# Kernel optimization log

Measured on AMD Instinct MI355X. Metric: run time of the kernel, lower is better.

The kernel has to match this reference:

```python
import jax, jax.numpy as jnp
from jax import lax
import numpy as np

B, T, H, A, C = 32, 4096, 512, 512, 32  # batch, enc frames, hidden, attn_size, conv_size


def setup_inputs() -> dict:
    key = jax.random.key(0)
    ks = jax.random.split(key, 10)
    return {
        "decoder_output": jax.random.normal(ks[0], (B, 1, H), jnp.float32),
        "encoder_outputs": jax.random.normal(ks[1], (B, T, H), jnp.float32),
        "last_alignment": jax.random.uniform(ks[2], (B, T), jnp.float32),
        "conv_w": jax.random.normal(ks[3], (C, 1, 3), jnp.float32) * 0.1,   # Conv1d(1->C, k=3)
        "conv_b": jax.random.normal(ks[4], (C,), jnp.float32) * 0.1,
        "W": jax.random.normal(ks[5], (A, H), jnp.float32) * (1.0 / np.sqrt(H)),
        "V": jax.random.normal(ks[6], (A, H), jnp.float32) * (1.0 / np.sqrt(H)),
        "U": jax.random.normal(ks[7], (A, C), jnp.float32) * (1.0 / np.sqrt(C)),
        "b": jax.random.uniform(ks[8], (A,), jnp.float32, -0.1, 0.1),
        "w": jax.random.normal(ks[9], (A,), jnp.float32) * (1.0 / np.sqrt(A)),
    }


def reference(decoder_output, encoder_outputs, last_alignment, conv_w, conv_b, W, V, U, b, w):
    # location conv: [B,1,T] -> [B,C,T], kernel 3, padding 1
    conv = lax.conv_general_dilated(
        last_alignment[:, None, :], conv_w,
        window_strides=(1,), padding=[(1, 1)],
        dimension_numbers=("NCH", "OIH", "NCH"))
    conv_feat = (conv + conv_b[None, :, None]).transpose(0, 2, 1)  # [B,T,C]

    dec_proj = jnp.einsum("blh,ah->bla", decoder_output, W)        # [B,1,A]
    enc_proj = jnp.einsum("bth,ah->bta", encoder_outputs, V)       # [B,T,A]
    loc_proj = jnp.einsum("btc,ac->bta", conv_feat, U)             # [B,T,A]

    scores = jnp.einsum("bta,a->bt", jnp.tanh(dec_proj + enc_proj + loc_proj + b), w)  # [B,T]
    alignment = jax.nn.softmax(scores, axis=-1)                    # [B,T]
    output = jnp.einsum("bt,bth->bh", alignment, encoder_outputs)  # [B,H]
    return output, alignment
```

## Files before the change

kernel.cpp:

```cpp
#include <hip/hip_runtime.h>
#include <hip/hip_bf16.h>

#define B_ 32
#define T_ 4096
#define H_ 512
#define A_ 512
#define C_ 32
#define KTOT 544
#define NKS  (KTOT / 32)
#define TT   64
#define NCH  (T_ / TT)

typedef float f32x4 __attribute__((ext_vector_type(4)));
typedef __bf16 bf16x8 __attribute__((ext_vector_type(8)));

__device__ inline float fast_tanh(float x) {
    float t = __expf(2.0f * x);
    return 1.0f - 2.0f / (t + 1.0f);
}

__device__ __forceinline__ void async16(const void* g, void* l) {
    __builtin_amdgcn_global_load_lds(
        (const __attribute__((address_space(1))) unsigned int*)g,
        (__attribute__((address_space(3))) unsigned int*)l, 16, 0, 0);
}

__global__ __launch_bounds__(256) void prep_kernel(
    const float* __restrict__ dec, const float* __restrict__ W,
    const float* __restrict__ bvec, const float* __restrict__ V,
    const float* __restrict__ U,
    float* __restrict__ dpb, __bf16* __restrict__ Vsall) {
    int id = blockIdx.x * 256 + threadIdx.x;
    const int N1 = B_ * A_;
    const int N2 = A_ * H_;
    if (id < N1) {
        int b = id / A_, a = id % A_;
        const float* dr = dec + b * H_;
        const float* wr = W + (size_t)a * H_;
        float s = 0.f;
        #pragma unroll 8
        for (int h = 0; h < H_; ++h) s += dr[h] * wr[h];
        dpb[id] = s + bvec[a];
    } else if (id < N1 + N2) {
        int e = id - N1;
        int a = e >> 9, k = e & 511;
        Vsall[((k >> 3) * A_ + a) * 8 + (k & 7)] = (__bf16)V[(size_t)a * H_ + k];
    } else {
        int e = id - N1 - N2;
        int a = e >> 5, c = e & 31;
        int k = H_ + c;
        Vsall[((k >> 3) * A_ + a) * 8 + (k & 7)] = (__bf16)U[a * C_ + c];
    }
}

__global__ __launch_bounds__(512) void scores_mfma(
    const float* __restrict__ enc, const float* __restrict__ align,
    const float* __restrict__ conv_w, const float* __restrict__ conv_b,
    const __bf16* __restrict__ Vsall, const float* __restrict__ dpb,
    const float* __restrict__ wvec, float* __restrict__ scores,
    float* __restrict__ ml_buf, float* __restrict__ u_buf) {
    const int bx = blockIdx.x;
    const int t0 = bx * TT;
    const int b  = blockIdx.y;
    const int tid = threadIdx.x;
    const int lane = tid & 63, wid = tid >> 6;
    const int row0 = lane & 15;
    const int kg   = lane >> 4;
    const int wq   = wid & 3;
    const int wr   = wid >> 2;
    const int wcol = wq * 128;

    __shared__ char smem[73728];
    float* spart = (float*)smem;
    float* eL    = (float*)(smem + 2048);
    float* mbox  = (float*)(smem + 2560);

    const float* encb = enc + ((size_t)b * T_ + t0) * H_;
    const int arow = tid >> 2, akgl = tid & 3;

    {
        __bf16* bdst = (__bf16*)(smem + 8192);
        #pragma unroll
        for (int i = 0; i < 4; ++i) {
            int u = i * 512 + tid;
            async16(Vsall + u * 8, bdst + u * 8);
        }
    }
    if (tid < 256) {
        const float* p = encb + arow * H_ + akgl * 8;
        f32x4 lo = *reinterpret_cast<const f32x4*>(p);
        f32x4 hi = *reinterpret_cast<const f32x4*>(p + 4);
        bf16x8 v;
        v[0] = (__bf16)lo.x; v[1] = (__bf16)lo.y; v[2] = (__bf16)lo.z; v[3] = (__bf16)lo.w;
        v[4] = (__bf16)hi.x; v[5] = (__bf16)hi.y; v[6] = (__bf16)hi.z; v[7] = (__bf16)hi.w;
        int g = tid ^ ((tid >> 4) & 7);
        *reinterpret_cast<bf16x8*>((__bf16*)smem + g * 8) = v;
    }
    __syncthreads();

    f32x4 acc[2][8];
    #pragma unroll
    for (int m = 0; m < 2; ++m)
        #pragma unroll
        for (int n = 0; n < 8; ++n) acc[m][n] = (f32x4){0.f, 0.f, 0.f, 0.f};

    int cur = 0;
    for (int ks = 0; ks < NKS; ++ks) {
        __bf16* Acur = (__bf16*)(smem + (cur ? 4096 : 0));
        __bf16* Anxt = (__bf16*)(smem + (cur ? 0 : 4096));
        __bf16* Bcur = (__bf16*)(smem + 8192 + (cur ? 32768 : 0));
        __bf16* Bnxt = (__bf16*)(smem + 8192 + (cur ? 0 : 32768));

        f32x4 alo, ahi;
        bool stage = (ks + 1 < NKS);
        bool conv_step = (ks + 1 == NKS - 1);
        if (stage) {
            const __bf16* vchunk = Vsall + (size_t)(ks + 1) * (4 * A_ * 8);
            #pragma unroll
            for (int i = 0; i < 4; ++i) {
                int u = i * 512 + tid;
                async16(vchunk + u * 8, Bnxt + u * 8);
            }
            if (tid < 256 && !conv_step) {
                const float* p = encb + arow * H_ + (ks + 1) * 32 + akgl * 8;
                alo = *reinterpret_cast<const f32x4*>(p);
                ahi = *reinterpret_cast<const f32x4*>(p + 4);
            }
        }

        bf16x8 afrag[2];
        #pragma unroll
        for (int m = 0; m < 2; ++m) {
            int row = wr * 32 + m * 16 + row0;
            int u = row * 4 + kg;
            int g = u ^ ((u >> 4) & 7);
            afrag[m] = *reinterpret_cast<const bf16x8*>(Acur + g * 8);
        }
        const __bf16* bp = Bcur + kg * (A_ * 8);
        #pragma unroll
        for (int n = 0; n < 8; ++n) {
            bf16x8 bfrag = *reinterpret_cast<const bf16x8*>(bp + (wcol + n * 16 + row0) * 8);
            acc[0][n] = __builtin_amdgcn_mfma_f32_16x16x32_bf16(afrag[0], bfrag, acc[0][n], 0, 0, 0);
            acc[1][n] = __builtin_amdgcn_mfma_f32_16x16x32_bf16(afrag[1], bfrag, acc[1][n], 0, 0, 0);
        }

        if (stage && tid < 256) {
            bf16x8 v;
            if (!conv_step) {
                v[0] = (__bf16)alo.x; v[1] = (__bf16)alo.y; v[2] = (__bf16)alo.z; v[3] = (__bf16)alo.w;
                v[4] = (__bf16)ahi.x; v[5] = (__bf16)ahi.y; v[6] = (__bf16)ahi.z; v[7] = (__bf16)ahi.w;
            } else {
                int t = t0 + arow;
                float x0 = (t > 0) ? align[b * T_ + t - 1] : 0.f;
                float x1 = align[b * T_ + t];
                float x2 = (t + 1 < T_) ? align[b * T_ + t + 1] : 0.f;
                #pragma unroll
                for (int e = 0; e < 8; ++e) {
                    int c = akgl * 8 + e;
                    v[e] = (__bf16)(conv_b[c] + conv_w[c * 3 + 0] * x0
                                  + conv_w[c * 3 + 1] * x1 + conv_w[c * 3 + 2] * x2);
                }
            }
            int g = tid ^ ((tid >> 4) & 7);
            *reinterpret_cast<bf16x8*>(Anxt + g * 8) = v;
        }
        __syncthreads();
        cur ^= 1;
    }

    float dval[8], wv[8];
    #pragma unroll
    for (int n = 0; n < 8; ++n) {
        int a = wcol + n * 16 + row0;
        dval[n] = dpb[b * A_ + a];
        wv[n]   = wvec[a];
    }
    #pragma unroll
    for (int m = 0; m < 2; ++m) {
        float rs[4] = {0.f, 0.f, 0.f, 0.f};
        #pragma unroll
        for (int n = 0; n < 8; ++n) {
            #pragma unroll
            for (int j = 0; j < 4; ++j) {
                float x = acc[m][n][j] + dval[n];
                rs[j] += fast_tanh(x) * wv[n];
            }
        }
        #pragma unroll
        for (int j = 0; j < 4; ++j) {
            float v = rs[j];
            v += __shfl_xor(v, 1);
            v += __shfl_xor(v, 2);
            v += __shfl_xor(v, 4);
            v += __shfl_xor(v, 8);
            if (row0 == 0) spart[wq * TT + wr * 32 + m * 16 + kg * 4 + j] = v;
        }
    }
    __syncthreads();

    if (tid < TT) {
        float s = spart[0 * TT + tid] + spart[1 * TT + tid]
                + spart[2 * TT + tid] + spart[3 * TT + tid];
        scores[b * T_ + t0 + tid] = s;
        float mx = s;
        #pragma unroll
        for (int off = 32; off >= 1; off >>= 1) mx = fmaxf(mx, __shfl_xor(mx, off));
        float e = __expf(s - mx);
        eL[tid] = e;
        float l = e;
        #pragma unroll
        for (int off = 32; off >= 1; off >>= 1) l += __shfl_xor(l, off);
        if (tid == 0) {
            mbox[0] = mx;
            ml_buf[((size_t)b * NCH + bx) * 2 + 0] = mx;
            ml_buf[((size_t)b * NCH + bx) * 2 + 1] = l;
        }
    }
    __syncthreads();
    {
        float u0 = 0.f, u1 = 0.f, u2 = 0.f, u3 = 0.f;
        const float* ep = encb + tid;
        #pragma unroll 4
        for (int t = 0; t < TT; t += 4) {
            u0 += eL[t]     * ep[(size_t)t * H_];
            u1 += eL[t + 1] * ep[(size_t)(t + 1) * H_];
            u2 += eL[t + 2] * ep[(size_t)(t + 2) * H_];
            u3 += eL[t + 3] * ep[(size_t)(t + 3) * H_];
        }
        u_buf[((size_t)b * NCH + bx) * H_ + tid] = (u0 + u1) + (u2 + u3);
    }
}

__global__ __launch_bounds__(256) void softmax_k(
    const float* __restrict__ scores, float* __restrict__ out_align) {
    int b = blockIdx.x;
    int tid = threadIdx.x;
    __shared__ float redm[4];
    __shared__ float reds[4];
    float local[16];
    float mx = -1e30f;
    #pragma unroll
    for (int i = 0; i < 16; ++i) {
        float s = scores[b * T_ + tid + i * 256];
        local[i] = s;
        mx = fmaxf(mx, s);
    }
    for (int off = 32; off >= 1; off >>= 1) mx = fmaxf(mx, __shfl_xor(mx, off));
    if ((tid & 63) == 0) redm[tid >> 6] = mx;
    __syncthreads();
    mx = fmaxf(fmaxf(redm[0], redm[1]), fmaxf(redm[2], redm[3]));
    float sum = 0.f;
    #pragma unroll
    for (int i = 0; i < 16; ++i) { local[i] = __expf(local[i] - mx); sum += local[i]; }
    for (int off = 32; off >= 1; off >>= 1) sum += __shfl_xor(sum, off);
    if ((tid & 63) == 0) reds[tid >> 6] = sum;
    __syncthreads();
    sum = reds[0] + reds[1] + reds[2] + reds[3];
    float inv = 1.0f / sum;
    #pragma unroll
    for (int i = 0; i < 16; ++i)
        out_align[b * T_ + tid + i * 256] = local[i] * inv;
}

__global__ __launch_bounds__(512) void combine2_k(
    const float* __restrict__ ml_buf, const float* __restrict__ u_buf,
    float* __restrict__ out) {
    int b = blockIdx.x;
    int h = threadIdx.x;
    __shared__ float wsh[NCH];
    __shared__ float dsh[1];
    if (h < NCH) {
        float m = ml_buf[((size_t)b * NCH + h) * 2];
        float mb = m;
        #pragma unroll
        for (int off = 32; off >= 1; off >>= 1) mb = fmaxf(mb, __shfl_xor(mb, off));
        float w = __expf(m - mb);
        wsh[h] = w;
        float d = w * ml_buf[((size_t)b * NCH + h) * 2 + 1];
        #pragma unroll
        for (int off = 32; off >= 1; off >>= 1) d += __shfl_xor(d, off);
        if (h == 0) dsh[0] = d;
    }
    __syncthreads();
    float acc = 0.f;
    #pragma unroll 4
    for (int c = 0; c < NCH; ++c)
        acc += wsh[c] * u_buf[((size_t)b * NCH + c) * H_ + h];
    out[b * H_ + h] = acc / dsh[0];
}

extern "C" void kernel_launch(void* const* d_in, const int* in_sizes, int n_in,
                              void* d_out, int out_size, void* d_ws, size_t ws_size,
                              hipStream_t stream) {
    const float* dec    = (const float*)d_in[0];
    const float* enc    = (const float*)d_in[1];
    const float* align  = (const float*)d_in[2];
    const float* conv_w = (const float*)d_in[3];
    const float* conv_b = (const float*)d_in[4];
    const float* W      = (const float*)d_in[5];
    const float* V      = (const float*)d_in[6];
    const float* U      = (const float*)d_in[7];
    const float* bvec   = (const float*)d_in[8];
    const float* wvec   = (const float*)d_in[9];
    float* out       = (float*)d_out;
    float* out_align = out + B_ * H_;

    char* ws = (char*)d_ws;
    float*  dpb    = (float*)(ws);
    float*  scores = (float*)(ws + (64 << 10));
    float*  ml_buf = (float*)(ws + (576 << 10));
    float*  u_buf  = (float*)(ws + (592 << 10));
    __bf16* Vsall  = (__bf16*)(ws + (592 << 10) + (4 << 20));

    prep_kernel<<<(B_ * A_ + A_ * H_ + A_ * C_) / 256, 256, 0, stream>>>(
        dec, W, bvec, V, U, dpb, Vsall);
    scores_mfma<<<dim3(T_ / TT, B_), 512, 0, stream>>>(enc, align, conv_w, conv_b,
                                                       Vsall, dpb, wvec, scores,
                                                       ml_buf, u_buf);
    softmax_k<<<B_, 256, 0, stream>>>(scores, out_align);
    combine2_k<<<B_, 512, 0, stream>>>(ml_buf, u_buf, out);
}
```

Before: 166.9 us.

## Keep all bf16 encoder tiles in LDS and reuse them for weighted sum

The A-tile staging buffers are no longer double-buffered. Each k-step's bf16 encoder slice now gets its own LDS region, so the whole 64x512 tile stays resident. The closing context accumulation reads encoder values from LDS instead of re-reading fp32 encoder rows from global memory. This removes a second global pass over the encoder block, but LDS per block grows to about 136KB, which cuts occupancy to one block per CU, and the context sum now uses bf16-rounded encoder values.

```diff
diff --git a/kernel.cpp b/kernel.cpp
--- a/kernel.cpp
+++ b/kernel.cpp
@@ -10,6 +10,11 @@
 #define NKS  (KTOT / 32)
 #define TT   64
 #define NCH  (T_ / TT)
+
+#define LDS_B0   69632
+#define LDS_SP   135168
+#define LDS_EL   136192
+#define LDS_SZ   136448
 
 typedef float f32x4 __attribute__((ext_vector_type(4)));
 typedef __bf16 bf16x8 __attribute__((ext_vector_type(8)));
@@ -70,16 +75,16 @@
     const int wr   = wid >> 2;
     const int wcol = wq * 128;
 
-    __shared__ char smem[73728];
-    float* spart = (float*)smem;
-    float* eL    = (float*)(smem + 2048);
-    float* mbox  = (float*)(smem + 2560);
+    __shared__ char smem[LDS_SZ];
+    float* spart = (float*)(smem + LDS_SP);
+    float* eL    = (float*)(smem + LDS_EL);
 
     const float* encb = enc + ((size_t)b * T_ + t0) * H_;
     const int arow = tid >> 2, akgl = tid & 3;
+    const int ag = tid ^ ((tid >> 4) & 7);
 
     {
-        __bf16* bdst = (__bf16*)(smem + 8192);
+        __bf16* bdst = (__bf16*)(smem + LDS_B0);
         #pragma unroll
         for (int i = 0; i < 4; ++i) {
             int u = i * 512 + tid;
@@ -93,8 +98,7 @@
         bf16x8 v;
         v[0] = (__bf16)lo.x; v[1] = (__bf16)lo.y; v[2] = (__bf16)lo.z; v[3] = (__bf16)lo.w;
         v[4] = (__bf16)hi.x; v[5] = (__bf16)hi.y; v[6] = (__bf16)hi.z; v[7] = (__bf16)hi.w;
-        int g = tid ^ ((tid >> 4) & 7);
-        *reinterpret_cast<bf16x8*>((__bf16*)smem + g * 8) = v;
+        *reinterpret_cast<bf16x8*>(smem + ag * 16) = v;
     }
     __syncthreads();
 
@@ -104,12 +108,11 @@
         #pragma unroll
         for (int n = 0; n < 8; ++n) acc[m][n] = (f32x4){0.f, 0.f, 0.f, 0.f};
 
-    int cur = 0;
     for (int ks = 0; ks < NKS; ++ks) {
-        __bf16* Acur = (__bf16*)(smem + (cur ? 4096 : 0));
-        __bf16* Anxt = (__bf16*)(smem + (cur ? 0 : 4096));
-        __bf16* Bcur = (__bf16*)(smem + 8192 + (cur ? 32768 : 0));
-        __bf16* Bnxt = (__bf16*)(smem + 8192 + (cur ? 0 : 32768));
+        char* Acur = smem + ks * 4096;
+        char* Anxt = smem + (ks + 1) * 4096;
+        char* Bcur = smem + LDS_B0 + (ks & 1) * 32768;
+        char* Bnxt = smem + LDS_B0 + ((ks + 1) & 1) * 32768;
 
         f32x4 alo, ahi;
         bool stage = (ks + 1 < NKS);
@@ -119,7 +122,7 @@
             #pragma unroll
             for (int i = 0; i < 4; ++i) {
                 int u = i * 512 + tid;
-                async16(vchunk + u * 8, Bnxt + u * 8);
+                async16(vchunk + u * 8, (__bf16*)Bnxt + u * 8);
             }
             if (tid < 256 && !conv_step) {
                 const float* p = encb + arow * H_ + (ks + 1) * 32 + akgl * 8;
@@ -134,9 +137,9 @@
             int row = wr * 32 + m * 16 + row0;
             int u = row * 4 + kg;
             int g = u ^ ((u >> 4) & 7);
-            afrag[m] = *reinterpret_cast<const bf16x8*>(Acur + g * 8);
-        }
-        const __bf16* bp = Bcur + kg * (A_ * 8);
+            afrag[m] = *reinterpret_cast<const bf16x8*>(Acur + g * 16);
+        }
+        const __bf16* bp = (const __bf16*)Bcur + kg * (A_ * 8);
         #pragma unroll
         for (int n = 0; n < 8; ++n) {
             bf16x8 bfrag = *reinterpret_cast<const bf16x8*>(bp + (wcol + n * 16 + row0) * 8);
@@ -161,11 +164,9 @@
                                   + conv_w[c * 3 + 1] * x1 + conv_w[c * 3 + 2] * x2);
                 }
             }
-            int g = tid ^ ((tid >> 4) & 7);
-            *reinterpret_cast<bf16x8*>(Anxt + g * 8) = v;
+            *reinterpret_cast<bf16x8*>(Anxt + ag * 16) = v;
         }
         __syncthreads();
-        cur ^= 1;
     }
 
     float dval[8], wv[8];
@@ -211,23 +212,28 @@
         #pragma unroll
         for (int off = 32; off >= 1; off >>= 1) l += __shfl_xor(l, off);
         if (tid == 0) {
-            mbox[0] = mx;
             ml_buf[((size_t)b * NCH + bx) * 2 + 0] = mx;
             ml_buf[((size_t)b * NCH + bx) * 2 + 1] = l;
         }
     }
     __syncthreads();
+
     {
-        float u0 = 0.f, u1 = 0.f, u2 = 0.f, u3 = 0.f;
-        const float* ep = encb + tid;
-        #pragma unroll 4
-        for (int t = 0; t < TT; t += 4) {
-            u0 += eL[t]     * ep[(size_t)t * H_];
-            u1 += eL[t + 1] * ep[(size_t)(t + 1) * H_];
-            u2 += eL[t + 2] * ep[(size_t)(t + 2) * H_];
-            u3 += eL[t + 3] * ep[(size_t)(t + 3) * H_];
-        }
-        u_buf[((size_t)b * NCH + bx) * H_ + tid] = (u0 + u1) + (u2 + u3);
+        const int ksh = tid >> 5;
+        const int kqh = (tid >> 3) & 3;
+        const int eh  = tid & 7;
+        const char* base = smem + ksh * 4096 + eh * 2;
+        float u0 = 0.f, u1 = 0.f;
+        #pragma unroll 8
+        for (int t = 0; t < TT; t += 2) {
+            int ua = t * 4 + kqh;
+            int ub = ua + 4;
+            int ga = ua ^ ((ua >> 4) & 7);
+            int gb = ub ^ ((ub >> 4) & 7);
+            u0 += eL[t]     * (float)(*(const __bf16*)(base + ga * 16));
+            u1 += eL[t + 1] * (float)(*(const __bf16*)(base + gb * 16));
+        }
+        u_buf[((size_t)b * NCH + bx) * H_ + tid] = u0 + u1;
     }
 }
 
```

New measurement: 211.0 us. 1.26x slower.
